# Kernel optimization log

Measured on AMD Instinct MI355X. Metric: run time of the kernel, lower is better.

Reference implementation:

```python
import jax, jax.numpy as jnp
import numpy as np

N_NODES = 100000
N_EDGES = 600000
D = 128
H = 256


def setup_inputs() -> dict:
    key = jax.random.key(0)
    ks = jax.random.split(key, 8)
    nodes = jax.random.normal(ks[0], (N_NODES, D), dtype=jnp.float32)
    senders = jax.random.randint(ks[1], (N_EDGES,), 0, N_NODES)
    receivers = jax.random.randint(ks[2], (N_EDGES,), 0, N_NODES)
    s = 0.05
    return {
        "nodes": nodes,
        "senders": senders,
        "receivers": receivers,
        "Wm1": jax.random.normal(ks[3], (D, H), dtype=jnp.float32) * s,
        "bm1": jnp.zeros((H,), dtype=jnp.float32),
        "Wm2": jax.random.normal(ks[4], (H, D), dtype=jnp.float32) * s,
        "bm2": jnp.zeros((D,), dtype=jnp.float32),
        "Wn1": jax.random.normal(ks[5], (2 * D, H), dtype=jnp.float32) * s,
        "bn1": jnp.zeros((H,), dtype=jnp.float32),
        "Wn2": jax.random.normal(ks[6], (H, D), dtype=jnp.float32) * s,
        "bn2": jnp.zeros((D,), dtype=jnp.float32),
    }


def reference(nodes, senders, receivers, Wm1, bm1, Wm2, bm2, Wn1, bn1, Wn2, bn2):
    # message MLP applied per node (vmap(message_fn) over nodes)
    m = jax.nn.relu(nodes @ Wm1 + bm1) @ Wm2 + bm2            # [N, D]
    # gather messages along edges by sender, segment_sum to receivers
    agg = jax.ops.segment_sum(m[senders], receivers, num_segments=nodes.shape[0])  # [N, D]
    # node update MLP on [nodes || aggregated messages]
    h = jnp.concatenate([nodes, agg], axis=-1)                # [N, 2D]
    upd = jax.nn.relu(h @ Wn1 + bn1) @ Wn2 + bn2              # [N, D]
    # residual add
    return nodes + upd
```

## Files before the change

### kernel.cpp

```cpp
#include <hip/hip_runtime.h>

#define NN 100000
#define DD 128
#define HH 256
#define NE 600000
#define CAP 32

typedef short bf8 __attribute__((ext_vector_type(8)));
typedef float f32x4 __attribute__((ext_vector_type(4)));
typedef unsigned short u16x8 __attribute__((ext_vector_type(8)));

__device__ __forceinline__ unsigned short f2bf(float f) {
  unsigned int u = __builtin_bit_cast(unsigned int, f);
  u += 0x7fffu + ((u >> 16) & 1u);
  return (unsigned short)(u >> 16);
}
__device__ __forceinline__ float bf2f(unsigned short h) {
  unsigned int u = ((unsigned int)h) << 16;
  return __builtin_bit_cast(float, u);
}

__global__ __launch_bounds__(256) void prep(
    const float* __restrict__ Wm1, const float* __restrict__ Wm2,
    const float* __restrict__ Wn1, const float* __restrict__ Wn2,
    unsigned short* __restrict__ Pm1, unsigned short* __restrict__ Pm2,
    unsigned short* __restrict__ Pn1, unsigned short* __restrict__ Pn2,
    int* __restrict__ cnt,
    const float* __restrict__ nodes, unsigned short* __restrict__ Xb,
    unsigned short* __restrict__ Mb) {
  int b = blockIdx.x;
  int gid = b * 256 + threadIdx.x;

  for (int i = gid; i < NN; i += 400 * 256) cnt[i] = 0;

  if (b == 399 && threadIdx.x < 16)
    *(u16x8*)(Mb + (size_t)NN * DD + threadIdx.x * 8) = (u16x8)0;

  for (int i = gid; i < NN * DD / 8; i += 400 * 256) {
    const float4 v0 = ((const float4*)nodes)[i * 2];
    const float4 v1 = ((const float4*)nodes)[i * 2 + 1];
    u16x8 o;
    o[0] = f2bf(v0.x); o[1] = f2bf(v0.y); o[2] = f2bf(v0.z); o[3] = f2bf(v0.w);
    o[4] = f2bf(v1.x); o[5] = f2bf(v1.y); o[6] = f2bf(v1.z); o[7] = f2bf(v1.w);
    ((u16x8*)Xb)[i] = o;
  }

  if (b < 80) {
    const float* W; unsigned short* P; int K, N, base;
    if (b < 16)      { W = Wm1; P = Pm1; K = 128; N = 256; base = 0;  }
    else if (b < 32) { W = Wm2; P = Pm2; K = 256; N = 128; base = 16; }
    else if (b < 64) { W = Wn1; P = Pn1; K = 256; N = 256; base = 32; }
    else             { W = Wn2; P = Pn2; K = 256; N = 128; base = 64; }
    int idx = (b - base) * 256 + threadIdx.x;
    int KT = K >> 5;
    int lane = idx & 63;
    int t = idx >> 6;
    int kt = t % KT, nt = t / KT;
    int n = nt * 16 + (lane & 15);
    int k0 = kt * 32 + (lane >> 4) * 8;
    unsigned short* dst = P + (size_t)idx * 8;
#pragma unroll
    for (int j = 0; j < 8; ++j) dst[j] = f2bf(W[(size_t)(k0 + j) * N + n]);
  }
}

__global__ __launch_bounds__(256) void msg_mlp(
    const unsigned short* __restrict__ Xb,
    const unsigned short* __restrict__ W1p, const float* __restrict__ b1,
    const unsigned short* __restrict__ W2p, const float* __restrict__ b2,
    unsigned short* __restrict__ Mb,
    const int* __restrict__ snd, const int* __restrict__ rcv,
    int* __restrict__ cnt, int* __restrict__ ebuf) {
  __shared__ __align__(16) unsigned short h[32][264];
  const int row0 = blockIdx.x * 32;
  const int tid = threadIdx.x;
  const int lane = tid & 63, wave = tid >> 6;
  const int l15 = lane & 15, l4 = lane >> 4;

  {
    int e = blockIdx.x * 256 + tid;
    if (e < NE) {
      int r = rcv[e];
      int pos = atomicAdd(&cnt[r], 1);
      if (pos < CAP) ebuf[r * CAP + pos] = snd[e];
    }
  }

#pragma unroll
  for (int i = 0; i < 2; ++i) {
    int flat = (i * 256 + tid) * 8;
    int r = flat >> 7, c = flat & 127;
    *(u16x8*)&h[r][c] = *(const u16x8*)(Xb + (size_t)(row0 + r) * DD + c);
  }
  __syncthreads();

  f32x4 acc[4][2];
#pragma unroll
  for (int mt = 0; mt < 4; ++mt)
#pragma unroll
    for (int nt = 0; nt < 2; ++nt) acc[mt][nt] = (f32x4){0.f, 0.f, 0.f, 0.f};
#pragma unroll
  for (int kt = 0; kt < 4; ++kt) {
    bf8 wfr[4], xfr[2];
#pragma unroll
    for (int mt = 0; mt < 4; ++mt) {
      int Htile = wave * 4 + mt;
      wfr[mt] = *(const bf8*)(W1p + ((size_t)(Htile * 4 + kt) * 64 + lane) * 8);
    }
#pragma unroll
    for (int nt = 0; nt < 2; ++nt)
      xfr[nt] = *(const bf8*)&h[nt * 16 + l15][kt * 32 + l4 * 8];
#pragma unroll
    for (int mt = 0; mt < 4; ++mt)
#pragma unroll
      for (int nt = 0; nt < 2; ++nt)
        acc[mt][nt] = __builtin_amdgcn_mfma_f32_16x16x32_bf16(wfr[mt], xfr[nt], acc[mt][nt], 0, 0, 0);
  }
  __syncthreads();

#pragma unroll
  for (int mt = 0; mt < 4; ++mt) {
    int Hbase = (wave * 4 + mt) * 16 + l4 * 4;
    float4 bv = *(const float4*)(b1 + Hbase);
#pragma unroll
    for (int nt = 0; nt < 2; ++nt) {
      ushort4 o;
      float v0 = acc[mt][nt][0] + bv.x; o.x = f2bf(v0 > 0.f ? v0 : 0.f);
      float v1 = acc[mt][nt][1] + bv.y; o.y = f2bf(v1 > 0.f ? v1 : 0.f);
      float v2 = acc[mt][nt][2] + bv.z; o.z = f2bf(v2 > 0.f ? v2 : 0.f);
      float v3 = acc[mt][nt][3] + bv.w; o.w = f2bf(v3 > 0.f ? v3 : 0.f);
      *(ushort4*)&h[nt * 16 + l15][Hbase] = o;
    }
  }
  __syncthreads();

  f32x4 acc2[2][2];
#pragma unroll
  for (int mt = 0; mt < 2; ++mt)
#pragma unroll
    for (int nt = 0; nt < 2; ++nt) acc2[mt][nt] = (f32x4){0.f, 0.f, 0.f, 0.f};
#pragma unroll
  for (int kt = 0; kt < 8; ++kt) {
    bf8 wfr[2], xfr[2];
#pragma unroll
    for (int mt = 0; mt < 2; ++mt) {
      int Dtile = wave * 2 + mt;
      wfr[mt] = *(const bf8*)(W2p + ((size_t)(Dtile * 8 + kt) * 64 + lane) * 8);
    }
#pragma unroll
    for (int nt = 0; nt < 2; ++nt)
      xfr[nt] = *(const bf8*)&h[nt * 16 + l15][kt * 32 + l4 * 8];
#pragma unroll
    for (int mt = 0; mt < 2; ++mt)
#pragma unroll
      for (int nt = 0; nt < 2; ++nt)
        acc2[mt][nt] = __builtin_amdgcn_mfma_f32_16x16x32_bf16(wfr[mt], xfr[nt], acc2[mt][nt], 0, 0, 0);
  }
#pragma unroll
  for (int mt = 0; mt < 2; ++mt) {
    int Dbase = (wave * 2 + mt) * 16 + l4 * 4;
    float4 bv = *(const float4*)(b2 + Dbase);
#pragma unroll
    for (int nt = 0; nt < 2; ++nt) {
      int node = row0 + nt * 16 + l15;
      ushort4 o;
      o.x = f2bf(acc2[mt][nt][0] + bv.x);
      o.y = f2bf(acc2[mt][nt][1] + bv.y);
      o.z = f2bf(acc2[mt][nt][2] + bv.z);
      o.w = f2bf(acc2[mt][nt][3] + bv.w);
      *(ushort4*)(Mb + (size_t)node * DD + Dbase) = o;
    }
  }
}

__global__ __launch_bounds__(256) void node_fused(
    const unsigned short* __restrict__ Xb, const unsigned short* __restrict__ Mb,
    const int* __restrict__ ebuf, const int* __restrict__ cnt,
    const unsigned short* __restrict__ W1p, const float* __restrict__ b1,
    const unsigned short* __restrict__ W2p, const float* __restrict__ b2,
    float* __restrict__ out) {
  __shared__ __align__(16) unsigned short h[32][264];
  const int row0 = blockIdx.x * 32;
  const int tid = threadIdx.x;
  const int lane = tid & 63, wave = tid >> 6;
  const int l15 = lane & 15, l4 = lane >> 4;
  const int halfid = lane >> 5, sub = lane & 31;

  int degv[4];
#pragma unroll
  for (int t = 0; t < 4; ++t) {
    int node = row0 + t * 8 + wave * 2 + halfid;
    int d = cnt[node];
    degv[t] = d < CAP ? d : CAP;
  }

  {
    int idx = tid * 4;
    int r = idx >> 5, s = idx & 31;
    *(int4*)(((int*)&h[r][128]) + s) = *(const int4*)(ebuf + (size_t)row0 * CAP + idx);
  }

#pragma unroll
  for (int i = 0; i < 2; ++i) {
    int flat = (i * 256 + tid) * 8;
    int r = flat >> 7, c = flat & 127;
    *(u16x8*)&h[r][c] = *(const u16x8*)(Xb + (size_t)(row0 + r) * DD + c);
  }
  __syncthreads();

#pragma unroll
  for (int t = 0; t < 4; ++t) {
    int ln = t * 8 + wave * 2 + halfid;
    int deg = degv[t];
    const int* sl_p = (const int*)&h[ln][128];
    float a0 = 0.f, a1 = 0.f, a2 = 0.f, a3 = 0.f;
    for (int bb = 0; bb < deg; bb += 8) {
      ushort4 mv[8];
#pragma unroll
      for (int u = 0; u < 8; ++u) {
        int s = sl_p[bb + u];
        int se = (bb + u < deg) ? s : NN;
        mv[u] = *(const ushort4*)(Mb + (size_t)se * DD + sub * 4);
      }
#pragma unroll
      for (int u = 0; u < 8; ++u) {
        a0 += bf2f(mv[u].x);
        a1 += bf2f(mv[u].y);
        a2 += bf2f(mv[u].z);
        a3 += bf2f(mv[u].w);
      }
    }
    ushort4 o;
    o.x = f2bf(a0); o.y = f2bf(a1); o.z = f2bf(a2); o.w = f2bf(a3);
    *(ushort4*)&h[ln][128 + sub * 4] = o;
  }
  __syncthreads();

  ushort4 resid[2][2];
#pragma unroll
  for (int mt = 0; mt < 2; ++mt)
#pragma unroll
    for (int nt = 0; nt < 2; ++nt)
      resid[mt][nt] = *(ushort4*)&h[nt * 16 + l15][(wave * 2 + mt) * 16 + l4 * 4];

  f32x4 acc[4][2];
#pragma unroll
  for (int mt = 0; mt < 4; ++mt)
#pragma unroll
    for (int nt = 0; nt < 2; ++nt) acc[mt][nt] = (f32x4){0.f, 0.f, 0.f, 0.f};
#pragma unroll
  for (int kt = 0; kt < 8; ++kt) {
    bf8 wfr[4], xfr[2];
#pragma unroll
    for (int mt = 0; mt < 4; ++mt) {
      int Htile = wave * 4 + mt;
      wfr[mt] = *(const bf8*)(W1p + ((size_t)(Htile * 8 + kt) * 64 + lane) * 8);
    }
#pragma unroll
    for (int nt = 0; nt < 2; ++nt)
      xfr[nt] = *(const bf8*)&h[nt * 16 + l15][kt * 32 + l4 * 8];
#pragma unroll
    for (int mt = 0; mt < 4; ++mt)
#pragma unroll
      for (int nt = 0; nt < 2; ++nt)
        acc[mt][nt] = __builtin_amdgcn_mfma_f32_16x16x32_bf16(wfr[mt], xfr[nt], acc[mt][nt], 0, 0, 0);
  }
  __syncthreads();

#pragma unroll
  for (int mt = 0; mt < 4; ++mt) {
    int Hbase = (wave * 4 + mt) * 16 + l4 * 4;
    float4 bv = *(const float4*)(b1 + Hbase);
#pragma unroll
    for (int nt = 0; nt < 2; ++nt) {
      ushort4 o;
      float v0 = acc[mt][nt][0] + bv.x; o.x = f2bf(v0 > 0.f ? v0 : 0.f);
      float v1 = acc[mt][nt][1] + bv.y; o.y = f2bf(v1 > 0.f ? v1 : 0.f);
      float v2 = acc[mt][nt][2] + bv.z; o.z = f2bf(v2 > 0.f ? v2 : 0.f);
      float v3 = acc[mt][nt][3] + bv.w; o.w = f2bf(v3 > 0.f ? v3 : 0.f);
      *(ushort4*)&h[nt * 16 + l15][Hbase] = o;
    }
  }
  __syncthreads();

  f32x4 acc2[2][2];
#pragma unroll
  for (int mt = 0; mt < 2; ++mt)
#pragma unroll
    for (int nt = 0; nt < 2; ++nt) acc2[mt][nt] = (f32x4){0.f, 0.f, 0.f, 0.f};
#pragma unroll
  for (int kt = 0; kt < 8; ++kt) {
    bf8 wfr[2], xfr[2];
#pragma unroll
    for (int mt = 0; mt < 2; ++mt) {
      int Dtile = wave * 2 + mt;
      wfr[mt] = *(const bf8*)(W2p + ((size_t)(Dtile * 8 + kt) * 64 + lane) * 8);
    }
#pragma unroll
    for (int nt = 0; nt < 2; ++nt)
      xfr[nt] = *(const bf8*)&h[nt * 16 + l15][kt * 32 + l4 * 8];
#pragma unroll
    for (int mt = 0; mt < 2; ++mt)
#pragma unroll
      for (int nt = 0; nt < 2; ++nt)
        acc2[mt][nt] = __builtin_amdgcn_mfma_f32_16x16x32_bf16(wfr[mt], xfr[nt], acc2[mt][nt], 0, 0, 0);
  }
#pragma unroll
  for (int mt = 0; mt < 2; ++mt) {
    int Dbase = (wave * 2 + mt) * 16 + l4 * 4;
    float4 bv = *(const float4*)(b2 + Dbase);
#pragma unroll
    for (int nt = 0; nt < 2; ++nt) {
      int node = row0 + nt * 16 + l15;
      float4 o;
      o.x = bf2f(resid[mt][nt].x) + acc2[mt][nt][0] + bv.x;
      o.y = bf2f(resid[mt][nt].y) + acc2[mt][nt][1] + bv.y;
      o.z = bf2f(resid[mt][nt].z) + acc2[mt][nt][2] + bv.z;
      o.w = bf2f(resid[mt][nt].w) + acc2[mt][nt][3] + bv.w;
      *(float4*)(out + (size_t)node * DD + Dbase) = o;
    }
  }
}

extern "C" void kernel_launch(void* const* d_in, const int* in_sizes, int n_in,
                              void* d_out, int out_size, void* d_ws, size_t ws_size,
                              hipStream_t stream) {
  const float* nodes = (const float*)d_in[0];
  const int* senders = (const int*)d_in[1];
  const int* receivers = (const int*)d_in[2];
  const float* Wm1 = (const float*)d_in[3];
  const float* bm1 = (const float*)d_in[4];
  const float* Wm2 = (const float*)d_in[5];
  const float* bm2 = (const float*)d_in[6];
  const float* Wn1 = (const float*)d_in[7];
  const float* bn1 = (const float*)d_in[8];
  const float* Wn2 = (const float*)d_in[9];
  const float* bn2 = (const float*)d_in[10];
  float* out = (float*)d_out;

  char* ws = (char*)d_ws;
  unsigned short* Mb   = (unsigned short*)(ws);
  unsigned short* Xb   = (unsigned short*)(ws + 25600512);
  int* cnt    = (int*)(ws + 51200512);
  int* ebuf   = (int*)(ws + 51600512);
  unsigned short* Wm1p = (unsigned short*)(ws + 64400512);
  unsigned short* Wm2p = (unsigned short*)(ws + 64466048);
  unsigned short* Wn1p = (unsigned short*)(ws + 64531584);
  unsigned short* Wn2p = (unsigned short*)(ws + 64662656);

  prep<<<400, 256, 0, stream>>>(Wm1, Wm2, Wn1, Wn2, Wm1p, Wm2p, Wn1p, Wn2p,
                                cnt, nodes, Xb, Mb);
  msg_mlp<<<3125, 256, 0, stream>>>(Xb, Wm1p, bm1, Wm2p, bm2, Mb,
                                    senders, receivers, cnt, ebuf);
  node_fused<<<3125, 256, 0, stream>>>(Xb, Mb, ebuf, cnt,
                                       Wn1p, bn1, Wn2p, bn2, out);
}
```

Before: 232.3 us.

## Store messages in fp8 and retile message MLP to 64-row blocks

Per-node messages are now stored as fp8 (e4m3) instead of bf16, which halves the bytes moved by the random gather in the aggregation step. The aggregation unpacks them with packed fp8-to-f32 conversions. The message MLP is also retiled to 512-thread blocks over 64 rows, with bounds guards for the last partial block, so each weight fragment is reused across more rows. The risk is accuracy: fp8 messages carry far less precision, and the error accumulates over summed edges.

```diff
diff --git a/kernel.cpp b/kernel.cpp
--- a/kernel.cpp
+++ b/kernel.cpp
@@ -8,6 +8,7 @@
 
 typedef short bf8 __attribute__((ext_vector_type(8)));
 typedef float f32x4 __attribute__((ext_vector_type(4)));
+typedef float f32x2 __attribute__((ext_vector_type(2)));
 typedef unsigned short u16x8 __attribute__((ext_vector_type(8)));
 
 __device__ __forceinline__ unsigned short f2bf(float f) {
@@ -27,14 +28,14 @@
     unsigned short* __restrict__ Pn1, unsigned short* __restrict__ Pn2,
     int* __restrict__ cnt,
     const float* __restrict__ nodes, unsigned short* __restrict__ Xb,
-    unsigned short* __restrict__ Mb) {
+    unsigned char* __restrict__ Mb) {
   int b = blockIdx.x;
   int gid = b * 256 + threadIdx.x;
 
   for (int i = gid; i < NN; i += 400 * 256) cnt[i] = 0;
 
-  if (b == 399 && threadIdx.x < 16)
-    *(u16x8*)(Mb + (size_t)NN * DD + threadIdx.x * 8) = (u16x8)0;
+  if (b == 399 && threadIdx.x < 8)
+    ((int4*)(Mb + (size_t)NN * DD))[threadIdx.x] = (int4){0, 0, 0, 0};
 
   for (int i = gid; i < NN * DD / 8; i += 400 * 256) {
     const float4 v0 = ((const float4*)nodes)[i * 2];
@@ -64,21 +65,21 @@
   }
 }
 
-__global__ __launch_bounds__(256) void msg_mlp(
+__global__ __launch_bounds__(512) void msg_mlp(
     const unsigned short* __restrict__ Xb,
     const unsigned short* __restrict__ W1p, const float* __restrict__ b1,
     const unsigned short* __restrict__ W2p, const float* __restrict__ b2,
-    unsigned short* __restrict__ Mb,
+    unsigned char* __restrict__ Mb,
     const int* __restrict__ snd, const int* __restrict__ rcv,
     int* __restrict__ cnt, int* __restrict__ ebuf) {
-  __shared__ __align__(16) unsigned short h[32][264];
-  const int row0 = blockIdx.x * 32;
+  __shared__ __align__(16) unsigned short h[64][264];
+  const int row0 = blockIdx.x * 64;
   const int tid = threadIdx.x;
   const int lane = tid & 63, wave = tid >> 6;
   const int l15 = lane & 15, l4 = lane >> 4;
 
   {
-    int e = blockIdx.x * 256 + tid;
+    int e = blockIdx.x * 512 + tid;
     if (e < NE) {
       int r = rcv[e];
       int pos = atomicAdd(&cnt[r], 1);
@@ -88,42 +89,44 @@
 
 #pragma unroll
   for (int i = 0; i < 2; ++i) {
-    int flat = (i * 256 + tid) * 8;
+    int flat = (i * 512 + tid) * 8;
     int r = flat >> 7, c = flat & 127;
-    *(u16x8*)&h[r][c] = *(const u16x8*)(Xb + (size_t)(row0 + r) * DD + c);
-  }
-  __syncthreads();
-
-  f32x4 acc[4][2];
-#pragma unroll
-  for (int mt = 0; mt < 4; ++mt)
-#pragma unroll
-    for (int nt = 0; nt < 2; ++nt) acc[mt][nt] = (f32x4){0.f, 0.f, 0.f, 0.f};
+    u16x8 v = (u16x8)0;
+    if (row0 + r < NN) v = *(const u16x8*)(Xb + (size_t)(row0 + r) * DD + c);
+    *(u16x8*)&h[r][c] = v;
+  }
+  __syncthreads();
+
+  f32x4 acc[2][4];
+#pragma unroll
+  for (int mt = 0; mt < 2; ++mt)
+#pragma unroll
+    for (int nt = 0; nt < 4; ++nt) acc[mt][nt] = (f32x4){0.f, 0.f, 0.f, 0.f};
 #pragma unroll
   for (int kt = 0; kt < 4; ++kt) {
-    bf8 wfr[4], xfr[2];
-#pragma unroll
-    for (int mt = 0; mt < 4; ++mt) {
-      int Htile = wave * 4 + mt;
+    bf8 wfr[2], xfr[4];
+#pragma unroll
+    for (int mt = 0; mt < 2; ++mt) {
+      int Htile = wave * 2 + mt;
       wfr[mt] = *(const bf8*)(W1p + ((size_t)(Htile * 4 + kt) * 64 + lane) * 8);
     }
 #pragma unroll
-    for (int nt = 0; nt < 2; ++nt)
+    for (int nt = 0; nt < 4; ++nt)
       xfr[nt] = *(const bf8*)&h[nt * 16 + l15][kt * 32 + l4 * 8];
 #pragma unroll
-    for (int mt = 0; mt < 4; ++mt)
-#pragma unroll
-      for (int nt = 0; nt < 2; ++nt)
+    for (int mt = 0; mt < 2; ++mt)
+#pragma unroll
+      for (int nt = 0; nt < 4; ++nt)
         acc[mt][nt] = __builtin_amdgcn_mfma_f32_16x16x32_bf16(wfr[mt], xfr[nt], acc[mt][nt], 0, 0, 0);
   }
   __syncthreads();
 
 #pragma unroll
-  for (int mt = 0; mt < 4; ++mt) {
-    int Hbase = (wave * 4 + mt) * 16 + l4 * 4;
+  for (int mt = 0; mt < 2; ++mt) {
+    int Hbase = wave * 32 + mt * 16 + l4 * 4;
     float4 bv = *(const float4*)(b1 + Hbase);
 #pragma unroll
-    for (int nt = 0; nt < 2; ++nt) {
+    for (int nt = 0; nt < 4; ++nt) {
       ushort4 o;
       float v0 = acc[mt][nt][0] + bv.x; o.x = f2bf(v0 > 0.f ? v0 : 0.f);
       float v1 = acc[mt][nt][1] + bv.y; o.y = f2bf(v1 > 0.f ? v1 : 0.f);
@@ -134,47 +137,38 @@
   }
   __syncthreads();
 
-  f32x4 acc2[2][2];
-#pragma unroll
-  for (int mt = 0; mt < 2; ++mt)
-#pragma unroll
-    for (int nt = 0; nt < 2; ++nt) acc2[mt][nt] = (f32x4){0.f, 0.f, 0.f, 0.f};
+  f32x4 acc2[4];
+#pragma unroll
+  for (int nt = 0; nt < 4; ++nt) acc2[nt] = (f32x4){0.f, 0.f, 0.f, 0.f};
 #pragma unroll
   for (int kt = 0; kt < 8; ++kt) {
-    bf8 wfr[2], xfr[2];
-#pragma unroll
-    for (int mt = 0; mt < 2; ++mt) {
-      int Dtile = wave * 2 + mt;
-      wfr[mt] = *(const bf8*)(W2p + ((size_t)(Dtile * 8 + kt) * 64 + lane) * 8);
-    }
-#pragma unroll
-    for (int nt = 0; nt < 2; ++nt)
+    bf8 wfr, xfr[4];
+    wfr = *(const bf8*)(W2p + ((size_t)(wave * 8 + kt) * 64 + lane) * 8);
+#pragma unroll
+    for (int nt = 0; nt < 4; ++nt)
       xfr[nt] = *(const bf8*)&h[nt * 16 + l15][kt * 32 + l4 * 8];
 #pragma unroll
-    for (int mt = 0; mt < 2; ++mt)
-#pragma unroll
-      for (int nt = 0; nt < 2; ++nt)
-        acc2[mt][nt] = __builtin_amdgcn_mfma_f32_16x16x32_bf16(wfr[mt], xfr[nt], acc2[mt][nt], 0, 0, 0);
-  }
-#pragma unroll
-  for (int mt = 0; mt < 2; ++mt) {
-    int Dbase = (wave * 2 + mt) * 16 + l4 * 4;
+    for (int nt = 0; nt < 4; ++nt)
+      acc2[nt] = __builtin_amdgcn_mfma_f32_16x16x32_bf16(wfr, xfr[nt], acc2[nt], 0, 0, 0);
+  }
+  {
+    int Dbase = wave * 16 + l4 * 4;
     float4 bv = *(const float4*)(b2 + Dbase);
 #pragma unroll
-    for (int nt = 0; nt < 2; ++nt) {
+    for (int nt = 0; nt < 4; ++nt) {
       int node = row0 + nt * 16 + l15;
-      ushort4 o;
-      o.x = f2bf(acc2[mt][nt][0] + bv.x);
-      o.y = f2bf(acc2[mt][nt][1] + bv.y);
-      o.z = f2bf(acc2[mt][nt][2] + bv.z);
-      o.w = f2bf(acc2[mt][nt][3] + bv.w);
-      *(ushort4*)(Mb + (size_t)node * DD + Dbase) = o;
+      if (node < NN) {
+        int p = 0;
+        p = __builtin_amdgcn_cvt_pk_fp8_f32(acc2[nt][0] + bv.x, acc2[nt][1] + bv.y, p, false);
+        p = __builtin_amdgcn_cvt_pk_fp8_f32(acc2[nt][2] + bv.z, acc2[nt][3] + bv.w, p, true);
+        *(unsigned int*)(Mb + (size_t)node * DD + Dbase) = (unsigned int)p;
+      }
     }
   }
 }
 
 __global__ __launch_bounds__(256) void node_fused(
-    const unsigned short* __restrict__ Xb, const unsigned short* __restrict__ Mb,
+    const unsigned short* __restrict__ Xb, const unsigned char* __restrict__ Mb,
     const int* __restrict__ ebuf, const int* __restrict__ cnt,
     const unsigned short* __restrict__ W1p, const float* __restrict__ b1,
     const unsigned short* __restrict__ W2p, const float* __restrict__ b2,
@@ -215,19 +209,18 @@
     const int* sl_p = (const int*)&h[ln][128];
     float a0 = 0.f, a1 = 0.f, a2 = 0.f, a3 = 0.f;
     for (int bb = 0; bb < deg; bb += 8) {
-      ushort4 mv[8];
+      unsigned int mv[8];
 #pragma unroll
       for (int u = 0; u < 8; ++u) {
         int s = sl_p[bb + u];
         int se = (bb + u < deg) ? s : NN;
-        mv[u] = *(const ushort4*)(Mb + (size_t)se * DD + sub * 4);
+        mv[u] = *(const unsigned int*)(Mb + (size_t)se * DD + sub * 4);
       }
 #pragma unroll
       for (int u = 0; u < 8; ++u) {
-        a0 += bf2f(mv[u].x);
-        a1 += bf2f(mv[u].y);
-        a2 += bf2f(mv[u].z);
-        a3 += bf2f(mv[u].w);
+        f32x2 lo = __builtin_amdgcn_cvt_pk_f32_fp8((int)mv[u], false);
+        f32x2 hi = __builtin_amdgcn_cvt_pk_f32_fp8((int)mv[u], true);
+        a0 += lo[0]; a1 += lo[1]; a2 += hi[0]; a3 += hi[1];
       }
     }
     ushort4 o;
@@ -339,18 +332,18 @@
   float* out = (float*)d_out;
 
   char* ws = (char*)d_ws;
-  unsigned short* Mb   = (unsigned short*)(ws);
-  unsigned short* Xb   = (unsigned short*)(ws + 25600512);
-  int* cnt    = (int*)(ws + 51200512);
-  int* ebuf   = (int*)(ws + 51600512);
-  unsigned short* Wm1p = (unsigned short*)(ws + 64400512);
-  unsigned short* Wm2p = (unsigned short*)(ws + 64466048);
-  unsigned short* Wn1p = (unsigned short*)(ws + 64531584);
-  unsigned short* Wn2p = (unsigned short*)(ws + 64662656);
+  unsigned char* Mb    = (unsigned char*)(ws);
+  unsigned short* Xb   = (unsigned short*)(ws + 12800256);
+  int* cnt    = (int*)(ws + 38400256);
+  int* ebuf   = (int*)(ws + 38800256);
+  unsigned short* Wm1p = (unsigned short*)(ws + 51600256);
+  unsigned short* Wm2p = (unsigned short*)(ws + 51665792);
+  unsigned short* Wn1p = (unsigned short*)(ws + 51731328);
+  unsigned short* Wn2p = (unsigned short*)(ws + 51862400);
 
   prep<<<400, 256, 0, stream>>>(Wm1, Wm2, Wn1, Wn2, Wm1p, Wm2p, Wn1p, Wn2p,
                                 cnt, nodes, Xb, Mb);
-  msg_mlp<<<3125, 256, 0, stream>>>(Xb, Wm1p, bm1, Wm2p, bm2, Mb,
+  msg_mlp<<<1563, 512, 0, stream>>>(Xb, Wm1p, bm1, Wm2p, bm2, Mb,
                                     senders, receivers, cnt, ebuf);
   node_fused<<<3125, 256, 0, stream>>>(Xb, Mb, ebuf, cnt,
                                        Wn1p, bn1, Wn2p, bn2, out);
```

After: 218.0 us. 6.2% less time.
